# Kernel optimization log

Hardware: AMD Instinct MI355X
Metric: run time of the kernel (lower is better)

## Reference

```python
import jax, jax.numpy as jnp
import numpy as np

N = 20000   # nodes
E = 320000  # edges (avg degree 16)
F = 8       # n_original_features (tokens per node)
D = 16      # embed_dim
H = 4       # num_heads
OUT = 7     # classes


def setup_inputs() -> dict:
    key = jax.random.key(0)
    ks = jax.random.split(key, 12)
    s = 0.1
    return {
        "x": jax.random.normal(ks[0], (N, F * D), dtype=jnp.float32),
        "edge_index": jax.random.randint(ks[1], (2, E), 0, N, dtype=jnp.int32),
        "conv1_wqkv": jax.random.normal(ks[2], (3 * D, D), dtype=jnp.float32) * s,
        "conv1_bqkv": jnp.zeros((3 * D,), dtype=jnp.float32),
        "conv1_wo": jax.random.normal(ks[3], (D, D), dtype=jnp.float32) * s,
        "conv1_bo": jnp.zeros((D,), dtype=jnp.float32),
        "conv2_wqkv": jax.random.normal(ks[4], (3 * D, D), dtype=jnp.float32) * s,
        "conv2_bqkv": jnp.zeros((3 * D,), dtype=jnp.float32),
        "conv2_wo": jax.random.normal(ks[5], (D, D), dtype=jnp.float32) * s,
        "conv2_bo": jnp.zeros((D,), dtype=jnp.float32),
        "out_w": jax.random.normal(ks[6], (OUT, F * D), dtype=jnp.float32) * s,
        "out_b": jnp.zeros((OUT,), dtype=jnp.float32),
    }


def _mha_edge(xq, xkv, wqkv, bqkv, wo, bo):
    # xq, xkv: [E, F, D]. torch MultiheadAttention: query=xq, key=value=xkv.
    dh = D // H
    wq, wk, wv = jnp.split(wqkv, 3, axis=0)
    bq, bk, bv = jnp.split(bqkv, 3)
    q = (xq @ wq.T + bq).reshape(-1, F, H, dh)
    k = (xkv @ wk.T + bk).reshape(-1, F, H, dh)
    v = (xkv @ wv.T + bv).reshape(-1, F, H, dh)
    scale = 1.0 / np.sqrt(dh).astype(np.float32)
    scores = jnp.einsum('efhd,eghd->ehfg', q, k) * scale  # [E,H,F,F]
    attn = jax.nn.softmax(scores, axis=-1)
    out = jnp.einsum('ehfg,eghd->efhd', attn, v).reshape(-1, F, D)
    return out @ wo.T + bo


def _amp_conv(x, src, dst, wqkv, bqkv, wo, bo):
    # gather per-edge token views; query = target node tokens (x_i), key/value = source (x_j)
    xj = x[src].reshape(-1, F, D)
    xi = x[dst].reshape(-1, F, D)
    msg = _mha_edge(xi, xj, wqkv, bqkv, wo, bo).reshape(-1, F * D)
    return jax.ops.segment_sum(msg, dst, num_segments=N)  # aggr='add' at targets


def reference(x, edge_index, conv1_wqkv, conv1_bqkv, conv1_wo, conv1_bo,
              conv2_wqkv, conv2_bqkv, conv2_wo, conv2_bo, out_w, out_b):
    src, dst = edge_index[0], edge_index[1]
    h = _amp_conv(x, src, dst, conv1_wqkv, conv1_bqkv, conv1_wo, conv1_bo)
    h = jax.nn.elu(h)
    h = _amp_conv(h, src, dst, conv2_wqkv, conv2_bqkv, conv2_wo, conv2_bo)
    h = jax.nn.elu(h)
    logits = h @ out_w.T + out_b
    return jax.nn.log_softmax(logits, axis=1)
```

## Files before the change

### kernel.cpp

```cpp
#include <hip/hip_runtime.h>
#include <hip/hip_bf16.h>
#include <math.h>

#define NN 20000
#define NE 320000
#define FT 8
#define DM 16
#define FD 128
#define OUTC 7
#define NFD (NN * FD)
#define CHK 20

typedef unsigned short ushort;
typedef unsigned int uint;
typedef __fp16 h2 __attribute__((ext_vector_type(2)));
union UH { uint u; h2 h; };

__device__ inline h2 u2h(uint x) { UH c; c.u = x; return c.h; }

__device__ inline float dot2(uint a, h2 b, float c) {
#if __has_builtin(__builtin_amdgcn_fdot2)
    return __builtin_amdgcn_fdot2(u2h(a), b, c, false);
#else
    h2 ah = u2h(a);
    return fmaf((float)ah.x, (float)b.x, fmaf((float)ah.y, (float)b.y, c));
#endif
}
__device__ inline float dot2u(uint a, uint b, float c) { return dot2(a, u2h(b), c); }

__device__ inline h2 pk(float a, float b) {
#if __has_builtin(__builtin_amdgcn_cvt_pkrtz)
    return __builtin_amdgcn_cvt_pkrtz(a, b);
#else
    h2 r; r.x = (__fp16)a; r.y = (__fp16)b; return r;
#endif
}
__device__ inline ushort f16b(float x) {
    union { __fp16 h; ushort u; } c; c.h = (__fp16)x; return c.u;
}
__device__ inline float rcpf(float x) {
#if __has_builtin(__builtin_amdgcn_rcpf)
    return __builtin_amdgcn_rcpf(x);
#else
    return 1.0f / x;
#endif
}
__device__ inline float exp2r(float x) {
#if __has_builtin(__builtin_amdgcn_exp2f)
    return __builtin_amdgcn_exp2f(x);
#else
    return exp2f(x);
#endif
}

#define QSCALE 0.7213475204444817f


__global__ __launch_bounds__(256) void qkv1_kernel(
    const float* __restrict__ x,
    const float* __restrict__ wqkv, const float* __restrict__ bqkv,
    ushort* __restrict__ qout, ushort* __restrict__ kvout) {
    __shared__ float sw[48 * 17];
    __shared__ float sb[48];
    __shared__ float sx[2][FD];
    __shared__ uint squ[2][64];
    __shared__ uint skvu[2][128];
    const int t = threadIdx.x;
    const int nh = t >> 7, tl = t & 127;
    const int n = blockIdx.x * 2 + nh;
    for (int i = t; i < 48 * 16; i += 256) sw[(i >> 4) * 17 + (i & 15)] = wqkv[i];
    if (t < 48) sb[t] = bqkv[t];
    sx[nh][tl] = x[(size_t)n * FD + tl];
    __syncthreads();
    const int f = tl >> 4, d = tl & 15, h = d >> 2, dd = d & 3;
    float aq = sb[d], ak = sb[16 + d], av = sb[32 + d];
    const float* xr = &sx[nh][f * 16];
#pragma unroll
    for (int e = 0; e < 16; ++e) {
        const float xe = xr[e];
        aq = fmaf(xe, sw[d * 17 + e], aq);
        ak = fmaf(xe, sw[(16 + d) * 17 + e], ak);
        av = fmaf(xe, sw[(32 + d) * 17 + e], av);
    }
    ushort* sq = (ushort*)squ[nh];
    ushort* skv = (ushort*)skvu[nh];
    sq[tl] = f16b(aq * QSCALE);
    skv[h * 64 + f * 4 + dd] = f16b(ak);
    skv[h * 64 + 32 + dd * 8 + f] = f16b(av);
    __syncthreads();
    if (tl < 64) ((uint*)(qout + (size_t)n * FD))[tl] = squ[nh][tl];
    ((uint*)(kvout + (size_t)n * 256))[tl] = skvu[nh][tl];
}

__global__ __launch_bounds__(256) void deg_kernel(const int* __restrict__ dst,
                                                  int* __restrict__ deg) {
    const int e = blockIdx.x * 256 + threadIdx.x;
    if (e < NE) atomicAdd(&deg[dst[e]], 1);
}

__global__ __launch_bounds__(1024) void scan_kernel(const int* __restrict__ deg,
                                                    int* __restrict__ rowstart,
                                                    int* __restrict__ cursor) {
    __shared__ int wsum[16];
    const int t = threadIdx.x;
    const int lane = t & 63, wid = t >> 6;
    const int base = t * CHK;
    int local[CHK];
    int s = 0;
#pragma unroll
    for (int i = 0; i < CHK; ++i) {
        const int idx = base + i;
        const int d = (idx < NN) ? deg[idx] : 0;
        local[i] = s;
        s += d;
    }
    int ws = s;
    for (int off = 1; off < 64; off <<= 1) {
        int tmp = __shfl_up(ws, off);
        if (lane >= off) ws += tmp;
    }
    if (lane == 63) wsum[wid] = ws;
    __syncthreads();
    if (wid == 0) {
        int v = (lane < 16) ? wsum[lane] : 0;
        for (int off = 1; off < 16; off <<= 1) {
            int tmp = __shfl_up(v, off);
            if (lane >= off) v += tmp;
        }
        if (lane < 16) wsum[lane] = v;
    }
    __syncthreads();
    const int excl = (ws - s) + (wid > 0 ? wsum[wid - 1] : 0);
#pragma unroll
    for (int i = 0; i < CHK; ++i) {
        const int idx = base + i;
        if (idx < NN) {
            const int v = excl + local[i];
            rowstart[idx] = v;
            cursor[idx] = v;
        }
    }
    if (t == 0) rowstart[NN] = NE;
}

__global__ __launch_bounds__(256) void scatter_kernel(
    const int* __restrict__ src, const int* __restrict__ dst,
    int* __restrict__ cursor, int* __restrict__ csr_src) {
    const int e = blockIdx.x * 256 + threadIdx.x;
    if (e < NE) {
        const int pos = atomicAdd(&cursor[dst[e]], 1);
        csr_src[pos] = src[e];
    }
}

__global__ __launch_bounds__(256) void edge_agg_kernel(
    const int* __restrict__ rowstart, const int* __restrict__ csr_src,
    const ushort* __restrict__ qh, const uint* __restrict__ kvw,
    float* __restrict__ accum) {
    const int w = (blockIdx.x * 256 + threadIdx.x) >> 6;
    if (w >= NN) return;
    const int lane = threadIdx.x & 63;
    const int slot = lane >> 2;
    const int h    = lane & 3;

    const uint* qrow = (const uint*)(qh + (size_t)w * FD);
    uint2 qp[8];
#pragma unroll
    for (int f = 0; f < 8; ++f)
        qp[f] = *(const uint2*)(qrow + f * 8 + h * 2);

    const int beg = rowstart[w], end = rowstart[w + 1];

    float acc[8][4];
#pragma unroll
    for (int f = 0; f < 8; ++f)
#pragma unroll
        for (int dd = 0; dd < 4; ++dd) acc[f][dd] = 0.f;

    int e = beg + slot;
    uint idx = (e < end) ? (uint)csr_src[e] : 0u;
    float gate = (e < end) ? 1.0f : 0.0f;

    for (int eb = beg; eb < end; eb += 16) {
        const uint4* p = (const uint4*)(kvw + (size_t)idx * 128 + h * 32);
        const uint4 k0 = p[0], k1 = p[1], k2 = p[2], k3 = p[3];
        const uint4 v0 = p[4], v1 = p[5], v2 = p[6], v3 = p[7];
        const int en = eb + 16 + slot;
        const uint idxn = (en < end) ? (uint)csr_src[en] : 0u;
        const float gaten = (en < end) ? 1.0f : 0.0f;

#pragma unroll
        for (int f = 0; f < 8; ++f) {
            const uint qx = qp[f].x, qy = qp[f].y;
            float s0 = dot2u(qy, k0.y, dot2u(qx, k0.x, 0.f));
            float s1 = dot2u(qy, k0.w, dot2u(qx, k0.z, 0.f));
            float s2 = dot2u(qy, k1.y, dot2u(qx, k1.x, 0.f));
            float s3 = dot2u(qy, k1.w, dot2u(qx, k1.z, 0.f));
            float s4 = dot2u(qy, k2.y, dot2u(qx, k2.x, 0.f));
            float s5 = dot2u(qy, k2.w, dot2u(qx, k2.z, 0.f));
            float s6 = dot2u(qy, k3.y, dot2u(qx, k3.x, 0.f));
            float s7 = dot2u(qy, k3.w, dot2u(qx, k3.z, 0.f));
            s0 = exp2r(s0); s1 = exp2r(s1); s2 = exp2r(s2); s3 = exp2r(s3);
            s4 = exp2r(s4); s5 = exp2r(s5); s6 = exp2r(s6); s7 = exp2r(s7);
            const float sum = ((s0 + s1) + (s2 + s3)) + ((s4 + s5) + (s6 + s7));
            const float inv = gate * rcpf(sum);
            const h2 e0 = pk(s0, s1), e1 = pk(s2, s3), e2 = pk(s4, s5), e3 = pk(s6, s7);
            const float p0 = dot2(v0.w, e3, dot2(v0.z, e2, dot2(v0.y, e1, dot2(v0.x, e0, 0.f))));
            const float p1 = dot2(v1.w, e3, dot2(v1.z, e2, dot2(v1.y, e1, dot2(v1.x, e0, 0.f))));
            const float p2 = dot2(v2.w, e3, dot2(v2.z, e2, dot2(v2.y, e1, dot2(v2.x, e0, 0.f))));
            const float p3 = dot2(v3.w, e3, dot2(v3.z, e2, dot2(v3.y, e1, dot2(v3.x, e0, 0.f))));
            acc[f][0] = fmaf(p0, inv, acc[f][0]);
            acc[f][1] = fmaf(p1, inv, acc[f][1]);
            acc[f][2] = fmaf(p2, inv, acc[f][2]);
            acc[f][3] = fmaf(p3, inv, acc[f][3]);
        }
        idx = idxn; gate = gaten;
    }

#pragma unroll
    for (int f = 0; f < 8; ++f)
#pragma unroll
        for (int dd = 0; dd < 4; ++dd) {
            float a = acc[f][dd];
            a += __shfl_xor(a, 4);
            a += __shfl_xor(a, 8);
            a += __shfl_xor(a, 16);
            a += __shfl_xor(a, 32);
            acc[f][dd] = a;
        }
    if (slot == 0) {
        float* arow = accum + (size_t)w * FD;
#pragma unroll
        for (int f = 0; f < 8; ++f)
            *(float4*)(arow + f * 16 + h * 4) =
                make_float4(acc[f][0], acc[f][1], acc[f][2], acc[f][3]);
    }
}

__global__ __launch_bounds__(256) void post_qkv_kernel(
    const float* __restrict__ accum, const int* __restrict__ deg,
    const float* __restrict__ wo, const float* __restrict__ bo,
    const float* __restrict__ wqkv, const float* __restrict__ bqkv,
    ushort* __restrict__ qout, ushort* __restrict__ kvout) {
    __shared__ float swo[16 * 17];
    __shared__ float sbo[16];
    __shared__ float swq[48 * 17];
    __shared__ float sbq[48];
    __shared__ float sa[2][FD];
    __shared__ float sh[2][FD];
    __shared__ uint squ[2][64];
    __shared__ uint skvu[2][128];
    const int t = threadIdx.x;
    const int nh = t >> 7, tl = t & 127;
    const int n = blockIdx.x * 2 + nh;
    for (int i = t; i < 16 * 16; i += 256) swo[(i >> 4) * 17 + (i & 15)] = wo[i];
    for (int i = t; i < 48 * 16; i += 256) swq[(i >> 4) * 17 + (i & 15)] = wqkv[i];
    if (t < 16) sbo[t] = bo[t];
    if (t < 48) sbq[t] = bqkv[t];
    sa[nh][tl] = accum[(size_t)n * FD + tl];
    __syncthreads();
    const int f = tl >> 4, d = tl & 15, h = d >> 2, dd = d & 3;
    float hv = (float)deg[n] * sbo[d];
#pragma unroll
    for (int e = 0; e < 16; ++e) hv = fmaf(sa[nh][f * 16 + e], swo[d * 17 + e], hv);
    hv = hv > 0.f ? hv : expm1f(hv);
    sh[nh][tl] = hv;
    __syncthreads();
    float aq = sbq[d], ak = sbq[16 + d], av = sbq[32 + d];
    const float* xr = &sh[nh][f * 16];
#pragma unroll
    for (int e = 0; e < 16; ++e) {
        const float xe = xr[e];
        aq = fmaf(xe, swq[d * 17 + e], aq);
        ak = fmaf(xe, swq[(16 + d) * 17 + e], ak);
        av = fmaf(xe, swq[(32 + d) * 17 + e], av);
    }
    ushort* sq = (ushort*)squ[nh];
    ushort* skv = (ushort*)skvu[nh];
    sq[tl] = f16b(aq * QSCALE);
    skv[h * 64 + f * 4 + dd] = f16b(ak);
    skv[h * 64 + 32 + dd * 8 + f] = f16b(av);
    __syncthreads();
    if (tl < 64) ((uint*)(qout + (size_t)n * FD))[tl] = squ[nh][tl];
    ((uint*)(kvout + (size_t)n * 256))[tl] = skvu[nh][tl];
}

__global__ __launch_bounds__(256) void post_cls_kernel(
    const float* __restrict__ accum, const int* __restrict__ deg,
    const float* __restrict__ wo, const float* __restrict__ bo,
    const float* __restrict__ cw, const float* __restrict__ cb,
    float* __restrict__ out) {
    __shared__ float swo[16 * 17];
    __shared__ float sbo[16];
    __shared__ float scw[OUTC * FD];
    __shared__ float sa[2][FD];
    __shared__ float sred[2][2][OUTC];
    const int t = threadIdx.x;
    const int nh = t >> 7, tl = t & 127;
    const int n = blockIdx.x * 2 + nh;
    for (int i = t; i < 16 * 16; i += 256) swo[(i >> 4) * 17 + (i & 15)] = wo[i];
    for (int i = t; i < OUTC * FD; i += 256) scw[i] = cw[i];
    if (t < 16) sbo[t] = bo[t];
    sa[nh][tl] = accum[(size_t)n * FD + tl];
    __syncthreads();
    const int f = tl >> 4, d = tl & 15;
    const int lane = t & 63, wid = (t >> 6) & 1;
    float hv = (float)deg[n] * sbo[d];
#pragma unroll
    for (int e = 0; e < 16; ++e) hv = fmaf(sa[nh][f * 16 + e], swo[d * 17 + e], hv);
    hv = hv > 0.f ? hv : expm1f(hv);
    float p[OUTC];
#pragma unroll
    for (int c = 0; c < OUTC; ++c) p[c] = hv * scw[c * FD + tl];
#pragma unroll
    for (int c = 0; c < OUTC; ++c)
        for (int off = 32; off; off >>= 1) p[c] += __shfl_xor(p[c], off);
    if (lane == 0)
#pragma unroll
        for (int c = 0; c < OUTC; ++c) sred[nh][wid][c] = p[c];
    __syncthreads();
    if (tl == 0) {
        float lg[OUTC];
        float m = -1e30f;
#pragma unroll
        for (int c = 0; c < OUTC; ++c) {
            lg[c] = sred[nh][0][c] + sred[nh][1][c] + cb[c];
            m = fmaxf(m, lg[c]);
        }
        float s = 0.f;
#pragma unroll
        for (int c = 0; c < OUTC; ++c) s += __expf(lg[c] - m);
        const float lse = m + logf(s);
#pragma unroll
        for (int c = 0; c < OUTC; ++c) out[(size_t)n * OUTC + c] = lg[c] - lse;
    }
}

extern "C" void kernel_launch(void* const* d_in, const int* in_sizes, int n_in,
                              void* d_out, int out_size, void* d_ws, size_t ws_size,
                              hipStream_t stream) {
    const float* x      = (const float*)d_in[0];
    const int*   ei     = (const int*)d_in[1];
    const float* w1qkv  = (const float*)d_in[2];
    const float* b1qkv  = (const float*)d_in[3];
    const float* w1o    = (const float*)d_in[4];
    const float* b1o    = (const float*)d_in[5];
    const float* w2qkv  = (const float*)d_in[6];
    const float* b2qkv  = (const float*)d_in[7];
    const float* w2o    = (const float*)d_in[8];
    const float* b2o    = (const float*)d_in[9];
    const float* outw   = (const float*)d_in[10];
    const float* outb   = (const float*)d_in[11];
    float* out = (float*)d_out;

    const int* srcp = ei;
    const int* dstp = ei + NE;

    ushort* qh    = (ushort*)d_ws;
    ushort* kvh   = qh + (size_t)NN * FD;
    float*  accum = (float*)(kvh + (size_t)NN * 256);
    int*    deg      = (int*)(accum + NFD);
    int*    rowstart = deg + NN;
    int*    cursor   = rowstart + NN + 1;
    int*    csr_src  = cursor + NN;

    (void)hipMemsetAsync(deg, 0, NN * sizeof(int), stream);
    deg_kernel<<<(NE + 255) / 256, 256, 0, stream>>>(dstp, deg);
    scan_kernel<<<1, 1024, 0, stream>>>(deg, rowstart, cursor);
    scatter_kernel<<<(NE + 255) / 256, 256, 0, stream>>>(srcp, dstp, cursor, csr_src);

    qkv1_kernel<<<NN / 2, 256, 0, stream>>>(x, w1qkv, b1qkv, qh, kvh);
    edge_agg_kernel<<<NN / 4, 256, 0, stream>>>(rowstart, csr_src, qh, (const uint*)kvh, accum);
    post_qkv_kernel<<<NN / 2, 256, 0, stream>>>(accum, deg, w1o, b1o, w2qkv, b2qkv, qh, kvh);
    edge_agg_kernel<<<NN / 4, 256, 0, stream>>>(rowstart, csr_src, qh, (const uint*)kvh, accum);
    post_cls_kernel<<<NN / 2, 256, 0, stream>>>(accum, deg, w2o, b2o, outw, outb, out);
}
```

Before: 232.6 us.

## Fuse output projection and next-layer QKV into edge aggregation; merge degree count into QKV1

```diff
diff --git a/kernel.cpp b/kernel.cpp
--- a/kernel.cpp
+++ b/kernel.cpp
@@ -8,8 +8,8 @@
 #define DM 16
 #define FD 128
 #define OUTC 7
-#define NFD (NN * FD)
 #define CHK 20
+#define DEGB 1250
 
 typedef unsigned short ushort;
 typedef unsigned int uint;
@@ -56,10 +56,16 @@
 #define QSCALE 0.7213475204444817f
 
 
-__global__ __launch_bounds__(256) void qkv1_kernel(
+__global__ __launch_bounds__(256) void qkv1_deg_kernel(
     const float* __restrict__ x,
     const float* __restrict__ wqkv, const float* __restrict__ bqkv,
+    const int* __restrict__ dst, int* __restrict__ deg,
     ushort* __restrict__ qout, ushort* __restrict__ kvout) {
+    if (blockIdx.x < DEGB) {
+        const int e = blockIdx.x * 256 + threadIdx.x;
+        if (e < NE) atomicAdd(&deg[dst[e]], 1);
+        return;
+    }
     __shared__ float sw[48 * 17];
     __shared__ float sb[48];
     __shared__ float sx[2][FD];
@@ -67,7 +73,7 @@
     __shared__ uint skvu[2][128];
     const int t = threadIdx.x;
     const int nh = t >> 7, tl = t & 127;
-    const int n = blockIdx.x * 2 + nh;
+    const int n = (blockIdx.x - DEGB) * 2 + nh;
     for (int i = t; i < 48 * 16; i += 256) sw[(i >> 4) * 17 + (i & 15)] = wqkv[i];
     if (t < 48) sb[t] = bqkv[t];
     sx[nh][tl] = x[(size_t)n * FD + tl];
@@ -90,12 +96,6 @@
     __syncthreads();
     if (tl < 64) ((uint*)(qout + (size_t)n * FD))[tl] = squ[nh][tl];
     ((uint*)(kvout + (size_t)n * 256))[tl] = skvu[nh][tl];
-}
-
-__global__ __launch_bounds__(256) void deg_kernel(const int* __restrict__ dst,
-                                                  int* __restrict__ deg) {
-    const int e = blockIdx.x * 256 + threadIdx.x;
-    if (e < NE) atomicAdd(&deg[dst[e]], 1);
 }
 
 __global__ __launch_bounds__(1024) void scan_kernel(const int* __restrict__ deg,
@@ -153,23 +153,41 @@
     }
 }
 
-__global__ __launch_bounds__(256) void edge_agg_kernel(
+template <int PHASE>
+__global__ __launch_bounds__(256) void edge_fused_kernel(
     const int* __restrict__ rowstart, const int* __restrict__ csr_src,
     const ushort* __restrict__ qh, const uint* __restrict__ kvw,
-    float* __restrict__ accum) {
-    const int w = (blockIdx.x * 256 + threadIdx.x) >> 6;
-    if (w >= NN) return;
-    const int lane = threadIdx.x & 63;
-    const int slot = lane >> 2;
-    const int h    = lane & 3;
-
-    const uint* qrow = (const uint*)(qh + (size_t)w * FD);
+    const float* __restrict__ wo, const float* __restrict__ bo,
+    const float* __restrict__ w2, const float* __restrict__ b2,
+    ushort* __restrict__ qout, ushort* __restrict__ kvout,
+    float* __restrict__ out) {
+    __shared__ float swb[1200];
+    __shared__ float srow[4][FD];
+    __shared__ uint spack[4][192];
+    const int t = threadIdx.x;
+    for (int i = t; i < 256; i += 256) swb[(i >> 4) * 17 + (i & 15)] = wo[i];
+    if (t < 16) swb[272 + t] = bo[t];
+    if (PHASE == 1) {
+        for (int i = t; i < 768; i += 256) swb[288 + (i >> 4) * 17 + (i & 15)] = w2[i];
+        if (t < 48) swb[1104 + t] = b2[t];
+    } else {
+        for (int i = t; i < OUTC * FD; i += 256) swb[288 + i] = w2[i];
+        if (t < OUTC) swb[1184 + t] = b2[t];
+    }
+    __syncthreads();
+
+    const int wv = t >> 6;
+    const int n = blockIdx.x * 4 + wv;
+    const int lane = t & 63;
+    const int slot = lane >> 2, h = lane & 3;
+
+    const uint* qrow = (const uint*)(qh + (size_t)n * FD);
     uint2 qp[8];
 #pragma unroll
     for (int f = 0; f < 8; ++f)
         qp[f] = *(const uint2*)(qrow + f * 8 + h * 2);
 
-    const int beg = rowstart[w], end = rowstart[w + 1];
+    const int beg = rowstart[n], end = rowstart[n + 1];
 
     float acc[8][4];
 #pragma unroll
@@ -229,110 +247,84 @@
             acc[f][dd] = a;
         }
     if (slot == 0) {
-        float* arow = accum + (size_t)w * FD;
 #pragma unroll
         for (int f = 0; f < 8; ++f)
-            *(float4*)(arow + f * 16 + h * 4) =
+            *(float4*)(&srow[wv][f * 16 + h * 4]) =
                 make_float4(acc[f][0], acc[f][1], acc[f][2], acc[f][3]);
     }
-}
-
-__global__ __launch_bounds__(256) void post_qkv_kernel(
-    const float* __restrict__ accum, const int* __restrict__ deg,
-    const float* __restrict__ wo, const float* __restrict__ bo,
-    const float* __restrict__ wqkv, const float* __restrict__ bqkv,
-    ushort* __restrict__ qout, ushort* __restrict__ kvout) {
-    __shared__ float swo[16 * 17];
-    __shared__ float sbo[16];
-    __shared__ float swq[48 * 17];
-    __shared__ float sbq[48];
-    __shared__ float sa[2][FD];
-    __shared__ float sh[2][FD];
-    __shared__ uint squ[2][64];
-    __shared__ uint skvu[2][128];
-    const int t = threadIdx.x;
-    const int nh = t >> 7, tl = t & 127;
-    const int n = blockIdx.x * 2 + nh;
-    for (int i = t; i < 16 * 16; i += 256) swo[(i >> 4) * 17 + (i & 15)] = wo[i];
-    for (int i = t; i < 48 * 16; i += 256) swq[(i >> 4) * 17 + (i & 15)] = wqkv[i];
-    if (t < 16) sbo[t] = bo[t];
-    if (t < 48) sbq[t] = bqkv[t];
-    sa[nh][tl] = accum[(size_t)n * FD + tl];
-    __syncthreads();
-    const int f = tl >> 4, d = tl & 15, h = d >> 2, dd = d & 3;
-    float hv = (float)deg[n] * sbo[d];
-#pragma unroll
-    for (int e = 0; e < 16; ++e) hv = fmaf(sa[nh][f * 16 + e], swo[d * 17 + e], hv);
-    hv = hv > 0.f ? hv : expm1f(hv);
-    sh[nh][tl] = hv;
-    __syncthreads();
-    float aq = sbq[d], ak = sbq[16 + d], av = sbq[32 + d];
-    const float* xr = &sh[nh][f * 16];
-#pragma unroll
-    for (int e = 0; e < 16; ++e) {
-        const float xe = xr[e];
-        aq = fmaf(xe, swq[d * 17 + e], aq);
-        ak = fmaf(xe, swq[(16 + d) * 17 + e], ak);
-        av = fmaf(xe, swq[(32 + d) * 17 + e], av);
-    }
-    ushort* sq = (ushort*)squ[nh];
-    ushort* skv = (ushort*)skvu[nh];
-    sq[tl] = f16b(aq * QSCALE);
-    skv[h * 64 + f * 4 + dd] = f16b(ak);
-    skv[h * 64 + 32 + dd * 8 + f] = f16b(av);
-    __syncthreads();
-    if (tl < 64) ((uint*)(qout + (size_t)n * FD))[tl] = squ[nh][tl];
-    ((uint*)(kvout + (size_t)n * 256))[tl] = skvu[nh][tl];
-}
-
-__global__ __launch_bounds__(256) void post_cls_kernel(
-    const float* __restrict__ accum, const int* __restrict__ deg,
-    const float* __restrict__ wo, const float* __restrict__ bo,
-    const float* __restrict__ cw, const float* __restrict__ cb,
-    float* __restrict__ out) {
-    __shared__ float swo[16 * 17];
-    __shared__ float sbo[16];
-    __shared__ float scw[OUTC * FD];
-    __shared__ float sa[2][FD];
-    __shared__ float sred[2][2][OUTC];
-    const int t = threadIdx.x;
-    const int nh = t >> 7, tl = t & 127;
-    const int n = blockIdx.x * 2 + nh;
-    for (int i = t; i < 16 * 16; i += 256) swo[(i >> 4) * 17 + (i & 15)] = wo[i];
-    for (int i = t; i < OUTC * FD; i += 256) scw[i] = cw[i];
-    if (t < 16) sbo[t] = bo[t];
-    sa[nh][tl] = accum[(size_t)n * FD + tl];
-    __syncthreads();
-    const int f = tl >> 4, d = tl & 15;
-    const int lane = t & 63, wid = (t >> 6) & 1;
-    float hv = (float)deg[n] * sbo[d];
-#pragma unroll
-    for (int e = 0; e < 16; ++e) hv = fmaf(sa[nh][f * 16 + e], swo[d * 17 + e], hv);
-    hv = hv > 0.f ? hv : expm1f(hv);
-    float p[OUTC];
-#pragma unroll
-    for (int c = 0; c < OUTC; ++c) p[c] = hv * scw[c * FD + tl];
-#pragma unroll
-    for (int c = 0; c < OUTC; ++c)
-        for (int off = 32; off; off >>= 1) p[c] += __shfl_xor(p[c], off);
-    if (lane == 0)
-#pragma unroll
-        for (int c = 0; c < OUTC; ++c) sred[nh][wid][c] = p[c];
-    __syncthreads();
-    if (tl == 0) {
-        float lg[OUTC];
-        float m = -1e30f;
-#pragma unroll
-        for (int c = 0; c < OUTC; ++c) {
-            lg[c] = sred[nh][0][c] + sred[nh][1][c] + cb[c];
-            m = fmaxf(m, lg[c]);
-        }
-        float s = 0.f;
-#pragma unroll
-        for (int c = 0; c < OUTC; ++c) s += __expf(lg[c] - m);
-        const float lse = m + logf(s);
-#pragma unroll
-        for (int c = 0; c < OUTC; ++c) out[(size_t)n * OUTC + c] = lg[c] - lse;
+    __syncthreads();
+
+    const int dgr = end - beg;
+    const int f0 = lane >> 4, d = lane & 15;
+    const float* swo = swb;
+    const float* sbo = swb + 272;
+    float hv0 = (float)dgr * sbo[d];
+    float hv1 = hv0;
+#pragma unroll
+    for (int ee = 0; ee < 16; ++ee) {
+        const float wde = swo[d * 17 + ee];
+        hv0 = fmaf(srow[wv][f0 * 16 + ee], wde, hv0);
+        hv1 = fmaf(srow[wv][(f0 + 4) * 16 + ee], wde, hv1);
+    }
+    hv0 = hv0 > 0.f ? hv0 : expm1f(hv0);
+    hv1 = hv1 > 0.f ? hv1 : expm1f(hv1);
+
+    if (PHASE == 1) {
+        __syncthreads();
+        srow[wv][lane] = hv0;
+        srow[wv][lane + 64] = hv1;
+        __syncthreads();
+        const float* swq = swb + 288;
+        const float* sbq = swb + 1104;
+        float aq0 = sbq[d], ak0 = sbq[16 + d], av0 = sbq[32 + d];
+        float aq1 = aq0, ak1 = ak0, av1 = av0;
+#pragma unroll
+        for (int ee = 0; ee < 16; ++ee) {
+            const float x0 = srow[wv][f0 * 16 + ee];
+            const float x1 = srow[wv][(f0 + 4) * 16 + ee];
+            const float wq = swq[d * 17 + ee];
+            const float wk = swq[(16 + d) * 17 + ee];
+            const float wvw = swq[(32 + d) * 17 + ee];
+            aq0 = fmaf(x0, wq, aq0); aq1 = fmaf(x1, wq, aq1);
+            ak0 = fmaf(x0, wk, ak0); ak1 = fmaf(x1, wk, ak1);
+            av0 = fmaf(x0, wvw, av0); av1 = fmaf(x1, wvw, av1);
+        }
+        ushort* sq = (ushort*)&spack[wv][0];
+        ushort* skv = (ushort*)&spack[wv][64];
+        const int hh = d >> 2, dd = d & 3;
+        sq[lane] = f16b(aq0 * QSCALE);
+        sq[lane + 64] = f16b(aq1 * QSCALE);
+        skv[hh * 64 + f0 * 4 + dd] = f16b(ak0);
+        skv[hh * 64 + (f0 + 4) * 4 + dd] = f16b(ak1);
+        skv[hh * 64 + 32 + dd * 8 + f0] = f16b(av0);
+        skv[hh * 64 + 32 + dd * 8 + f0 + 4] = f16b(av1);
+        __syncthreads();
+        ((uint*)(qout + (size_t)n * FD))[lane] = spack[wv][lane];
+        uint* kvo = (uint*)(kvout + (size_t)n * 256);
+        kvo[lane] = spack[wv][64 + lane];
+        kvo[lane + 64] = spack[wv][128 + lane];
+    } else {
+        const float* scw = swb + 288;
+        const float* scb = swb + 1184;
+        float p[OUTC];
+#pragma unroll
+        for (int c = 0; c < OUTC; ++c)
+            p[c] = fmaf(hv0, scw[c * FD + lane], hv1 * scw[c * FD + lane + 64]);
+#pragma unroll
+        for (int c = 0; c < OUTC; ++c)
+            for (int off = 32; off; off >>= 1) p[c] += __shfl_xor(p[c], off);
+        if (lane == 0) {
+            float lg[OUTC];
+            float m = -1e30f;
+#pragma unroll
+            for (int c = 0; c < OUTC; ++c) { lg[c] = p[c] + scb[c]; m = fmaxf(m, lg[c]); }
+            float s = 0.f;
+#pragma unroll
+            for (int c = 0; c < OUTC; ++c) s += __expf(lg[c] - m);
+            const float lse = m + logf(s);
+#pragma unroll
+            for (int c = 0; c < OUTC; ++c) out[(size_t)n * OUTC + c] = lg[c] - lse;
+        }
     }
 }
 
@@ -358,20 +350,22 @@
 
     ushort* qh    = (ushort*)d_ws;
     ushort* kvh   = qh + (size_t)NN * FD;
-    float*  accum = (float*)(kvh + (size_t)NN * 256);
-    int*    deg      = (int*)(accum + NFD);
+    ushort* qh2   = kvh + (size_t)NN * 256;
+    ushort* kvh2  = qh2 + (size_t)NN * FD;
+    int*    deg      = (int*)(kvh2 + (size_t)NN * 256);
     int*    rowstart = deg + NN;
     int*    cursor   = rowstart + NN + 1;
     int*    csr_src  = cursor + NN;
 
     (void)hipMemsetAsync(deg, 0, NN * sizeof(int), stream);
-    deg_kernel<<<(NE + 255) / 256, 256, 0, stream>>>(dstp, deg);
+    qkv1_deg_kernel<<<DEGB + NN / 2, 256, 0, stream>>>(x, w1qkv, b1qkv, dstp, deg, qh, kvh);
     scan_kernel<<<1, 1024, 0, stream>>>(deg, rowstart, cursor);
     scatter_kernel<<<(NE + 255) / 256, 256, 0, stream>>>(srcp, dstp, cursor, csr_src);
 
-    qkv1_kernel<<<NN / 2, 256, 0, stream>>>(x, w1qkv, b1qkv, qh, kvh);
-    edge_agg_kernel<<<NN / 4, 256, 0, stream>>>(rowstart, csr_src, qh, (const uint*)kvh, accum);
-    post_qkv_kernel<<<NN / 2, 256, 0, stream>>>(accum, deg, w1o, b1o, w2qkv, b2qkv, qh, kvh);
-    edge_agg_kernel<<<NN / 4, 256, 0, stream>>>(rowstart, csr_src, qh, (const uint*)kvh, accum);
-    post_cls_kernel<<<NN / 2, 256, 0, stream>>>(accum, deg, w2o, b2o, outw, outb, out);
-}
+    edge_fused_kernel<1><<<NN / 4, 256, 0, stream>>>(
+        rowstart, csr_src, qh, (const uint*)kvh, w1o, b1o, w2qkv, b2qkv,
+        qh2, kvh2, nullptr);
+    edge_fused_kernel<2><<<NN / 4, 256, 0, stream>>>(
+        rowstart, csr_src, qh2, (const uint*)kvh2, w2o, b2o, outw, outb,
+        nullptr, nullptr, out);
+}
```

After: 207.4 us. -10.8%, faster.
